# Optimization experiments

Hardware: AMD Instinct MI355X
Metric: run time of the kernel (lower is better)

The kernel has to match this reference:

```python
import jax, jax.numpy as jnp
import numpy as np

B, E, H, W = 8, 1024, 16, 1024
DH = E // H


def setup_inputs() -> dict:
    key = jax.random.key(0)
    ks = jax.random.split(key, 5)
    scale = E ** (-0.5)
    return {
        "x": jax.random.normal(ks[0], (3, B, E, W), dtype=jnp.float32),
        "L_Q": jax.random.normal(ks[1], (E, E), dtype=jnp.float32) * scale,
        "L_K": jax.random.normal(ks[2], (E, E), dtype=jnp.float32) * scale,
        "L_V": jax.random.normal(ks[3], (E, E), dtype=jnp.float32) * scale,
        "dense_M": jax.random.normal(ks[4], (E, E), dtype=jnp.float32) * scale,
        "dense_b": jnp.zeros((E, 1), dtype=jnp.float32),
    }


def reference(x, L_Q, L_K, L_V, dense_M, dense_b):
    # x: [3, B, E, W], channels-first sequences (dropout layers are identity in eval)
    K, Q, V = x[0], x[1], x[2]                      # each [B, E, W]
    K = jnp.einsum('ef,bfw->bew', L_K, K)
    Q = jnp.einsum('ef,bfw->bew', L_Q, Q)
    V = jnp.einsum('ef,bfw->bew', L_V, V)
    Kv = K.reshape(B, H, DH, W)
    Qv = Q.reshape(B, H, DH, W)
    Vv = V.reshape(B, H, DH, W)
    # Q_v^T @ K_v -> [B, H, Wq, Wk]
    scores = jnp.einsum('bhdq,bhdk->bhqk', Qv, Kv)
    # causal_factor = tril(-inf, diag=-1): -inf strictly below the diagonal (q > k)
    qi = jnp.arange(W)[:, None]
    ki = jnp.arange(W)[None, :]
    scores = jnp.where(qi > ki, -jnp.inf, scores)
    # softmax over the QUERY axis (-2), post-scaled by E^-0.5 (non-standard)
    attn = jax.nn.softmax(scores, axis=-2) * (E ** (-0.5))
    # V_v @ scores: contract over the query axis -> [B, H, DH, Wk]
    out = jnp.einsum('bhdq,bhqk->bhdk', Vv, attn).reshape(B, E, W)
    # dense output projection: M @ out + b (bias broadcasts over W)
    return jnp.einsum('ef,bfw->bew', dense_M, out) + dense_b
```

## Files before the change

### kernel.cpp

```cpp
#include <hip/hip_runtime.h>

typedef float  f4  __attribute__((ext_vector_type(4)));
typedef short  s8v __attribute__((ext_vector_type(8)));
typedef unsigned short u16;
typedef u16 us4 __attribute__((ext_vector_type(4)));

constexpr int En  = 1024;
constexpr int Wn  = 1024;
constexpr int Bn  = 8;
constexpr int Hn  = 16;
constexpr int DHn = 64;

__device__ inline u16 bf16rn(float x) {
    unsigned u = __float_as_uint(x);
    return (u16)((u + 0x7FFFu + ((u >> 16) & 1u)) >> 16);
}
__device__ inline float bf16tof(u16 h) { return __uint_as_float(((unsigned)h) << 16); }

#define GLD_LDS16(gp, lp) __builtin_amdgcn_global_load_lds(                      \
    (const __attribute__((address_space(1))) void*)(gp),                         \
    (__attribute__((address_space(3))) void*)(lp), 16, 0, 0)

__global__ void split_plain4(const float* __restrict__ p0,
                             const float* __restrict__ p1,
                             const float* __restrict__ p2,
                             const float* __restrict__ p3,
                             u16* __restrict__ base) {
    const int z = blockIdx.y;
    const float* in = (z == 0) ? p0 : (z == 1) ? p1 : (z == 2) ? p2 : p3;
    u16* hi = base + (size_t)(2 * z) * En * En;
    u16* lo = base + (size_t)(2 * z + 1) * En * En;
    int i = blockIdx.x * blockDim.x + threadIdx.x;
    f4 v = ((const f4*)in)[i];
    us4 h, l;
    #pragma unroll
    for (int k = 0; k < 4; ++k) {
        u16 hh = bf16rn(v[k]);
        h[k] = hh;
        l[k] = bf16rn(v[k] - bf16tof(hh));
    }
    ((us4*)hi)[i] = h;
    ((us4*)lo)[i] = l;
}

__global__ __launch_bounds__(256)
void split_t(const float* __restrict__ in, u16* __restrict__ hi,
             u16* __restrict__ lo) {
    __shared__ float T[32][33];
    const int z = blockIdx.z;
    const size_t zo = (size_t)z * En * Wn;
    const int r0 = blockIdx.y * 32, c0 = blockIdx.x * 32;
    const int t = threadIdx.x;
    const int row = t >> 3, c4 = (t & 7) << 2;

    f4 v = *(const f4*)&in[zo + (size_t)(r0 + row) * Wn + c0 + c4];
    T[row][c4 + 0] = v[0]; T[row][c4 + 1] = v[1];
    T[row][c4 + 2] = v[2]; T[row][c4 + 3] = v[3];
    __syncthreads();

    const int oc = row, r4 = c4;
    us4 h, l;
    #pragma unroll
    for (int i = 0; i < 4; ++i) {
        float x = T[r4 + i][oc];
        u16 hh = bf16rn(x);
        h[i] = hh;
        l[i] = bf16rn(x - bf16tof(hh));
    }
    *(us4*)&hi[zo + (size_t)(c0 + oc) * En + r0 + r4] = h;
    *(us4*)&lo[zo + (size_t)(c0 + oc) * En + r0 + r4] = l;
}

template<int MODE>
__global__ __launch_bounds__(256, 3)
void gemm_mfma(const u16* __restrict__ Ah,  const u16* __restrict__ Al,
               const u16* __restrict__ Bth, const u16* __restrict__ Btl,
               float* __restrict__ Yf, u16* __restrict__ Yh, u16* __restrict__ Yl,
               const float* __restrict__ bias) {
    __shared__ u16 AsH[4096], AsL[4096], BsH[4096], BsL[4096];

    const int z  = blockIdx.z;
    const size_t zB = (size_t)z * Wn * En;
    const int e0 = blockIdx.y * 128, n0 = blockIdx.x * 128;
    const int t = threadIdx.x, lane = t & 63, wave = t >> 6;
    const int q = lane >> 4, r = lane & 15;
    const int m_off = (wave & 1) * 64, n_off = (wave >> 1) * 64;

    f4 acc[4][4];
    #pragma unroll
    for (int i = 0; i < 4; ++i)
        #pragma unroll
        for (int j = 0; j < 4; ++j) { acc[i][j][0]=0; acc[i][j][1]=0; acc[i][j][2]=0; acc[i][j][3]=0; }

    for (int kb = 0; kb < En; kb += 32) {
        __syncthreads();
        #pragma unroll
        for (int it = 0; it < 2; ++it) {
            const int id = t + 256 * it;
            const int u = id >> 3;
            const int p = (id & 7) ^ (u & 7);
            const int m = 2 * u + (p >> 2), g = p & 3;
            const size_t colA = (size_t)kb + 8 * g;
            const u16* ga_h = Ah  + (size_t)(e0 + m) * En + colA;
            const u16* ga_l = Al  + (size_t)(e0 + m) * En + colA;
            const u16* gb_h = Bth + zB + (size_t)(n0 + m) * En + colA;
            const u16* gb_l = Btl + zB + (size_t)(n0 + m) * En + colA;
            GLD_LDS16(ga_h, &AsH[id * 8]);
            GLD_LDS16(ga_l, &AsL[id * 8]);
            GLD_LDS16(gb_h, &BsH[id * 8]);
            GLD_LDS16(gb_l, &BsL[id * 8]);
        }
        __syncthreads();

        s8v aH[4], aL[4];
        #pragma unroll
        for (int i = 0; i < 4; ++i) {
            const int Ra = m_off + 16 * i + r;
            const int sa = ((((Ra & 1) << 2) | q) ^ ((Ra >> 1) & 7));
            const int ai = ((Ra >> 1) * 8 + sa) * 8;
            aH[i] = *(const s8v*)&AsH[ai];
            aL[i] = *(const s8v*)&AsL[ai];
        }
        #pragma unroll
        for (int j = 0; j < 4; ++j) {
            const int Rb = n_off + 16 * j + r;
            const int sb = ((((Rb & 1) << 2) | q) ^ ((Rb >> 1) & 7));
            const int bi = ((Rb >> 1) * 8 + sb) * 8;
            s8v bH = *(const s8v*)&BsH[bi];
            s8v bL = *(const s8v*)&BsL[bi];
            #pragma unroll
            for (int i = 0; i < 4; ++i) {
                acc[i][j] = __builtin_amdgcn_mfma_f32_16x16x32_bf16(aH[i], bH, acc[i][j], 0, 0, 0);
                acc[i][j] = __builtin_amdgcn_mfma_f32_16x16x32_bf16(aH[i], bL, acc[i][j], 0, 0, 0);
                acc[i][j] = __builtin_amdgcn_mfma_f32_16x16x32_bf16(aL[i], bH, acc[i][j], 0, 0, 0);
            }
        }
    }

    if constexpr (MODE == 0) {
        const size_t zY = (size_t)z * En * Wn;
        #pragma unroll
        for (int i = 0; i < 4; ++i) {
            #pragma unroll
            for (int reg = 0; reg < 4; ++reg) {
                const int e = e0 + m_off + 16 * i + q * 4 + reg;
                const float bv = bias ? bias[e] : 0.0f;
                #pragma unroll
                for (int j = 0; j < 4; ++j) {
                    const int w = n0 + n_off + 16 * j + r;
                    Yf[zY + (size_t)e * Wn + w] = acc[i][j][reg] + bv;
                }
            }
        }
    }
    if constexpr (MODE == 1) {
        #pragma unroll
        for (int i = 0; i < 4; ++i) {
            const int e_base = e0 + m_off + 16 * i + q * 4;
            const int bh_e = z * Hn + (e_base >> 6);
            const int d0 = e_base & 63;
            #pragma unroll
            for (int j = 0; j < 4; ++j) {
                const int w = n0 + n_off + 16 * j + r;
                us4 h, l;
                #pragma unroll
                for (int reg = 0; reg < 4; ++reg) {
                    float x = acc[i][j][reg];
                    u16 hh = bf16rn(x);
                    h[reg] = hh;
                    l[reg] = bf16rn(x - bf16tof(hh));
                }
                const size_t o = ((size_t)bh_e * Wn + w) * 64 + d0;
                *(us4*)&Yh[o] = h;
                *(us4*)&Yl[o] = l;
            }
        }
    }
    if constexpr (MODE == 2) {
        #pragma unroll
        for (int i = 0; i < 4; ++i) {
            #pragma unroll
            for (int reg = 0; reg < 4; ++reg) {
                const int e = e0 + m_off + 16 * i + q * 4 + reg;
                const int bh_e = z * Hn + (e >> 6);
                const int d = e & 63;
                const size_t ro = ((size_t)bh_e * 64 + d) * Wn;
                #pragma unroll
                for (int j = 0; j < 4; ++j) {
                    const int w = n0 + n_off + 16 * j + r;
                    Yh[ro + w] = bf16rn(acc[i][j][reg]);
                }
            }
        }
    }
}

__global__ __launch_bounds__(256, 3)
void attn_mfma3(const u16* __restrict__ QTh, const u16* __restrict__ QTl,
                const u16* __restrict__ KTh, const u16* __restrict__ KTl,
                const u16* __restrict__ Vb,  u16* __restrict__ AoTh,
                u16* __restrict__ AoTl) {
    __shared__ u16 QsH[4096], QsL[4096], Vs[4096];
    __shared__ u16 PT[4][16][72];

    const int id   = blockIdx.x;
    const int rest = id >> 3;
    const int kb   = 15 - (rest & 15);
    const int bh   = (id & 7) + 8 * (rest >> 4);

    const int t = threadIdx.x, lane = t & 63, wave = t >> 6;
    const int r = lane & 15, quad = lane >> 4;
    const int k0 = kb * 64;
    const int kcol = k0 + wave * 16 + r;
    u16 (*pt)[72] = PT[wave];

    const size_t qkb = (size_t)bh * Wn * 64;
    const size_t vbb = (size_t)bh * 64 * Wn;

    s8v kH[2], kL[2];
    #pragma unroll
    for (int s = 0; s < 2; ++s) {
        const size_t a = qkb + (size_t)kcol * 64 + s * 32 + quad * 8;
        kH[s] = *(const s8v*)&KTh[a];
        kL[s] = *(const s8v*)&KTl[a];
    }

    f4 o[4];
    #pragma unroll
    for (int i = 0; i < 4; ++i) { o[i][0]=0; o[i][1]=0; o[i][2]=0; o[i][3]=0; }
    float m = -1e30f, l = 0.0f;

    const int c0 = t,       row0 = c0 >> 3, p0 = (c0 & 7) ^ (row0 & 7);
    const int c1 = t + 256, row1 = c1 >> 3, p1 = (c1 & 7) ^ (row1 & 7);

    s8v Aqh0, Aqh1, Aql0, Aql1, Av0, Av1;
    s8v Bqh0, Bqh1, Bql0, Bql1, Bv0, Bv1;

    auto ld = [&](int q0, s8v& qh0, s8v& qh1, s8v& ql0, s8v& ql1,
                  s8v& v0, s8v& v1) {
        const size_t g = qkb + (size_t)q0 * 64;
        qh0 = *(const s8v*)&QTh[g + (size_t)row0 * 64 + p0 * 8];
        ql0 = *(const s8v*)&QTl[g + (size_t)row0 * 64 + p0 * 8];
        v0  = *(const s8v*)&Vb[vbb + (size_t)row0 * Wn + q0 + p0 * 8];
        qh1 = *(const s8v*)&QTh[g + (size_t)row1 * 64 + p1 * 8];
        ql1 = *(const s8v*)&QTl[g + (size_t)row1 * 64 + p1 * 8];
        v1  = *(const s8v*)&Vb[vbb + (size_t)row1 * Wn + q0 + p1 * 8];
    };
    auto wr = [&](s8v& qh0, s8v& qh1, s8v& ql0, s8v& ql1, s8v& v0, s8v& v1) {
        *(s8v*)&QsH[c0 * 8] = qh0; *(s8v*)&QsL[c0 * 8] = ql0; *(s8v*)&Vs[c0 * 8] = v0;
        *(s8v*)&QsH[c1 * 8] = qh1; *(s8v*)&QsL[c1 * 8] = ql1; *(s8v*)&Vs[c1 * 8] = v1;
    };

    auto compute = [&](int q0) {
        f4 sacc[4];
        #pragma unroll
        for (int mt = 0; mt < 4; ++mt) { sacc[mt][0]=0; sacc[mt][1]=0; sacc[mt][2]=0; sacc[mt][3]=0; }
        #pragma unroll
        for (int s = 0; s < 2; ++s) {
            const int sw = (((s * 4 + quad) ^ (r & 7)) << 3);
            #pragma unroll
            for (int mt = 0; mt < 4; ++mt) {
                const int a = (16 * mt + r) * 64 + sw;
                s8v qh = *(const s8v*)&QsH[a];
                s8v ql = *(const s8v*)&QsL[a];
                sacc[mt] = __builtin_amdgcn_mfma_f32_16x16x32_bf16(qh, kH[s], sacc[mt], 0, 0, 0);
                sacc[mt] = __builtin_amdgcn_mfma_f32_16x16x32_bf16(qh, kL[s], sacc[mt], 0, 0, 0);
                sacc[mt] = __builtin_amdgcn_mfma_f32_16x16x32_bf16(ql, kH[s], sacc[mt], 0, 0, 0);
            }
        }
        if (q0 == k0) {
            const int klocal = wave * 16 + r;
            #pragma unroll
            for (int mt = 0; mt < 4; ++mt)
                #pragma unroll
                for (int reg = 0; reg < 4; ++reg)
                    if (16 * mt + quad * 4 + reg > klocal) sacc[mt][reg] = -1e30f;
        }
        float tm = -1e30f;
        #pragma unroll
        for (int mt = 0; mt < 4; ++mt)
            #pragma unroll
            for (int reg = 0; reg < 4; ++reg) tm = fmaxf(tm, sacc[mt][reg]);
        tm = fmaxf(tm, __shfl_xor(tm, 16));
        tm = fmaxf(tm, __shfl_xor(tm, 32));
        if (!__all(tm - m <= 8.0f)) {
            const float mnew  = fmaxf(m, tm);
            const float alpha = __expf(m - mnew);
            l *= alpha;
            #pragma unroll
            for (int i = 0; i < 4; ++i) {
                o[i][0] *= alpha; o[i][1] *= alpha;
                o[i][2] *= alpha; o[i][3] *= alpha;
            }
            m = mnew;
        }
        float ps = 0.0f;
        #pragma unroll
        for (int mt = 0; mt < 4; ++mt) {
            us4 pk;
            #pragma unroll
            for (int reg = 0; reg < 4; ++reg) {
                float p = __expf(sacc[mt][reg] - m);
                ps += p;
                pk[reg] = bf16rn(p);
            }
            *(us4*)&pt[r][16 * mt + quad * 4] = pk;
        }
        ps += __shfl_xor(ps, 16);
        ps += __shfl_xor(ps, 32);
        l += ps;
        #pragma unroll
        for (int s = 0; s < 2; ++s) {
            const int sw = (((s * 4 + quad) ^ (r & 7)) << 3);
            s8v pf = *(const s8v*)&pt[r][s * 32 + quad * 8];
            #pragma unroll
            for (int i = 0; i < 4; ++i) {
                s8v vf = *(const s8v*)&Vs[(16 * i + r) * 64 + sw];
                o[i] = __builtin_amdgcn_mfma_f32_16x16x32_bf16(vf, pf, o[i], 0, 0, 0);
            }
        }
    };

    ld(0, Aqh0, Aqh1, Aql0, Aql1, Av0, Av1);
    int q0 = 0;
    for (;;) {
        __syncthreads();
        wr(Aqh0, Aqh1, Aql0, Aql1, Av0, Av1);
        __syncthreads();
        if (q0 + 64 <= k0) ld(q0 + 64, Bqh0, Bqh1, Bql0, Bql1, Bv0, Bv1);
        compute(q0);
        q0 += 64;
        if (q0 > k0) break;
        __syncthreads();
        wr(Bqh0, Bqh1, Bql0, Bql1, Bv0, Bv1);
        __syncthreads();
        if (q0 + 64 <= k0) ld(q0 + 64, Aqh0, Aqh1, Aql0, Aql1, Av0, Av1);
        compute(q0);
        q0 += 64;
        if (q0 > k0) break;
    }

    const float inv = 1.0f / (l * 32.0f);
    const size_t ob0 = (size_t)(bh >> 4) * ((size_t)Wn * En) +
                       (size_t)kcol * En + (bh & 15) * 64 + quad * 4;
    #pragma unroll
    for (int i = 0; i < 4; ++i) {
        us4 h, lo4;
        #pragma unroll
        for (int reg = 0; reg < 4; ++reg) {
            float x = o[i][reg] * inv;
            u16 hh = bf16rn(x);
            h[reg] = hh;
            lo4[reg] = bf16rn(x - bf16tof(hh));
        }
        *(us4*)&AoTh[ob0 + 16 * i] = h;
        *(us4*)&AoTl[ob0 + 16 * i] = lo4;
    }
}

__global__ __launch_bounds__(256, 2)
void gemm128(const float* __restrict__ L, const float* __restrict__ X,
             float* __restrict__ Y, const float* __restrict__ bias) {
    __shared__ float As[16][132];
    __shared__ float Bs[16][132];

    const int bz = blockIdx.z;
    const float* Xb = X + (size_t)bz * En * Wn;
    float*       Yb = Y + (size_t)bz * En * Wn;
    const int e0 = blockIdx.y * 128;
    const int w0 = blockIdx.x * 128;
    const int t  = threadIdx.x;
    const int tx = t & 15, ty = t >> 4;
    const int la_e = t >> 2, la_f = (t & 3) << 2;
    const int lb_f = t >> 5, lb_w = (t & 31) << 2;

    float acc[2][2][4][4] = {};

    for (int f0 = 0; f0 < En; f0 += 16) {
        f4 a0 = *(const f4*)&L [(size_t)(e0 + la_e)      * En + f0 + la_f];
        f4 a1 = *(const f4*)&L [(size_t)(e0 + la_e + 64) * En + f0 + la_f];
        f4 b0 = *(const f4*)&Xb[(size_t)(f0 + lb_f)      * Wn + w0 + lb_w];
        f4 b1 = *(const f4*)&Xb[(size_t)(f0 + lb_f + 8)  * Wn + w0 + lb_w];
        __syncthreads();
        As[la_f + 0][la_e] = a0[0]; As[la_f + 1][la_e] = a0[1];
        As[la_f + 2][la_e] = a0[2]; As[la_f + 3][la_e] = a0[3];
        As[la_f + 0][la_e + 64] = a1[0]; As[la_f + 1][la_e + 64] = a1[1];
        As[la_f + 2][la_e + 64] = a1[2]; As[la_f + 3][la_e + 64] = a1[3];
        *(f4*)&Bs[lb_f    ][lb_w] = b0;
        *(f4*)&Bs[lb_f + 8][lb_w] = b1;
        __syncthreads();
        #pragma unroll
        for (int kk = 0; kk < 16; ++kk) {
            f4 av0 = *(f4*)&As[kk][ty * 4];
            f4 av1 = *(f4*)&As[kk][ty * 4 + 64];
            f4 bv0 = *(f4*)&Bs[kk][tx * 4];
            f4 bv1 = *(f4*)&Bs[kk][tx * 4 + 64];
            #pragma unroll
            for (int i = 0; i < 4; ++i)
                #pragma unroll
                for (int j = 0; j < 4; ++j) {
                    acc[0][0][i][j] = fmaf(av0[i], bv0[j], acc[0][0][i][j]);
                    acc[0][1][i][j] = fmaf(av0[i], bv1[j], acc[0][1][i][j]);
                    acc[1][0][i][j] = fmaf(av1[i], bv0[j], acc[1][0][i][j]);
                    acc[1][1][i][j] = fmaf(av1[i], bv1[j], acc[1][1][i][j]);
                }
        }
    }

    #pragma unroll
    for (int eh = 0; eh < 2; ++eh)
        #pragma unroll
        for (int i = 0; i < 4; ++i) {
            const int e = e0 + eh * 64 + ty * 4 + i;
            const float bv = bias ? bias[e] : 0.0f;
            #pragma unroll
            for (int wh = 0; wh < 2; ++wh) {
                f4 v;
                #pragma unroll
                for (int j = 0; j < 4; ++j) v[j] = acc[eh][wh][i][j] + bv;
                *(f4*)&Yb[(size_t)e * Wn + w0 + wh * 64 + tx * 4] = v;
            }
        }
}

__global__ __launch_bounds__(256, 2)
void attn64(const float* __restrict__ Qg, const float* __restrict__ Kg,
            const float* __restrict__ Vg, float* __restrict__ Og) {
    __shared__ float Ks[64][68];
    __shared__ float QP[64][68];
    __shared__ float Vt[64][68];
    __shared__ float mArr[64], lArr[64], alphaArr[64];
    __shared__ float red[4][64];

    const int kb = blockIdx.x, h = blockIdx.y, b = blockIdx.z;
    const size_t base = ((size_t)b * En + (size_t)h * DHn) * Wn;
    const float* Qp = Qg + base;
    const float* Kp = Kg + base;
    const float* Vp = Vg + base;
    float*       Op = Og + base;

    const int t  = threadIdx.x;
    const int tx = t & 15, ty = t >> 4;
    const int lr = t >> 4;
    const int lc = (t & 15) << 2;
    const int k0 = kb * 64;
    const int kc = t & 63, qg = t >> 6;

    #pragma unroll
    for (int r = 0; r < 4; ++r)
        *(f4*)&Ks[lr + r * 16][lc] =
            *(const f4*)&Kp[(size_t)(lr + r * 16) * Wn + k0 + lc];
    if (t < 64) { mArr[t] = -1e30f; lArr[t] = 0.0f; }
    float acc[4][4] = {};
    __syncthreads();

    for (int q0 = 0; q0 <= k0; q0 += 64) {
        #pragma unroll
        for (int r = 0; r < 4; ++r) {
            const int d = lr + r * 16;
            f4 qv = *(const f4*)&Qp[(size_t)d * Wn + q0 + lc];
            f4 vv = *(const f4*)&Vp[(size_t)d * Wn + q0 + lc];
            *(f4*)&QP[d][lc] = qv;
            Vt[lc + 0][d] = vv[0]; Vt[lc + 1][d] = vv[1];
            Vt[lc + 2][d] = vv[2]; Vt[lc + 3][d] = vv[3];
        }
        __syncthreads();

        float s[4][4] = {};
        #pragma unroll 4
        for (int d = 0; d < 64; ++d) {
            f4 kv = *(f4*)&Ks[d][tx * 4];
            f4 q2 = *(f4*)&QP[d][ty * 4];
            #pragma unroll
            for (int i = 0; i < 4; ++i)
                #pragma unroll
                for (int j = 0; j < 4; ++j)
                    s[i][j] = fmaf(q2[i], kv[j], s[i][j]);
        }
        if (q0 == k0) {
            #pragma unroll
            for (int i = 0; i < 4; ++i)
                #pragma unroll
                for (int j = 0; j < 4; ++j)
                    if (ty * 4 + i > tx * 4 + j) s[i][j] = -1e30f;
        }
        __syncthreads();
        #pragma unroll
        for (int i = 0; i < 4; ++i) {
            f4 v;
            #pragma unroll
            for (int j = 0; j < 4; ++j) v[j] = s[i][j];
            *(f4*)&QP[ty * 4 + i][tx * 4] = v;
        }
        __syncthreads();

        float sv[16];
        float lm = -1e30f;
        #pragma unroll
        for (int r = 0; r < 16; ++r) {
            sv[r] = QP[qg * 16 + r][kc];
            lm = fmaxf(lm, sv[r]);
        }
        red[qg][kc] = lm;
        __syncthreads();
        const float mt    = fmaxf(fmaxf(red[0][kc], red[1][kc]),
                                  fmaxf(red[2][kc], red[3][kc]));
        const float mprev = mArr[kc];
        const float mnew  = fmaxf(mprev, mt);
        float psum = 0.0f;
        #pragma unroll
        for (int r = 0; r < 16; ++r) {
            const float p = __expf(sv[r] - mnew);
            psum += p;
            QP[qg * 16 + r][kc] = p;
        }
        __syncthreads();
        red[qg][kc] = psum;
        __syncthreads();
        if (qg == 0) {
            const float alpha = __expf(mprev - mnew);
            lArr[kc] = lArr[kc] * alpha +
                       (red[0][kc] + red[1][kc] + red[2][kc] + red[3][kc]);
            mArr[kc]     = mnew;
            alphaArr[kc] = alpha;
        }
        __syncthreads();

        f4 al = *(f4*)&alphaArr[tx * 4];
        #pragma unroll
        for (int i = 0; i < 4; ++i)
            #pragma unroll
            for (int j = 0; j < 4; ++j)
                acc[i][j] *= al[j];
        #pragma unroll 4
        for (int q = 0; q < 64; ++q) {
            f4 pv = *(f4*)&QP[q][tx * 4];
            f4 v2 = *(f4*)&Vt[q][ty * 4];
            #pragma unroll
            for (int i = 0; i < 4; ++i)
                #pragma unroll
                for (int j = 0; j < 4; ++j)
                    acc[i][j] = fmaf(v2[i], pv[j], acc[i][j]);
        }
        __syncthreads();
    }

    f4 linv = *(f4*)&lArr[tx * 4];
    #pragma unroll
    for (int j = 0; j < 4; ++j) linv[j] = 1.0f / (linv[j] * 32.0f);
    #pragma unroll
    for (int i = 0; i < 4; ++i) {
        f4 v;
        #pragma unroll
        for (int j = 0; j < 4; ++j) v[j] = acc[i][j] * linv[j];
        *(f4*)&Op[(size_t)(ty * 4 + i) * Wn + k0 + tx * 4] = v;
    }
}

extern "C" void kernel_launch(void* const* d_in, const int* in_sizes, int n_in,
                              void* d_out, int out_size, void* d_ws, size_t ws_size,
                              hipStream_t stream) {
    const float* x    = (const float*)d_in[0];
    const float* L_Q  = (const float*)d_in[1];
    const float* L_K  = (const float*)d_in[2];
    const float* L_V  = (const float*)d_in[3];
    const float* M    = (const float*)d_in[4];
    const float* bias = (const float*)d_in[5];
    float* out = (float*)d_out;

    const size_t mat   = (size_t)Bn * En * Wn;
    const size_t matB  = mat * 4;
    const size_t lmatB = (size_t)En * En * 2;
    const size_t need  = 8 * lmatB + 4 * matB + matB / 2 + matB;

    if (ws_size >= need) {
        char* w = (char*)d_ws;
        u16*  Lsp = (u16*)w;
        char* XT  = w + 8 * lmatB;
        char* R1  = XT + matB;
        char* R2  = R1 + matB;
        char* R3  = R2 + matB;
        char* R4  = R3 + matB / 2;

        u16* LKh = Lsp + 0 * (lmatB / 2); u16* LKl = Lsp + 1 * (lmatB / 2);
        u16* LQh = Lsp + 2 * (lmatB / 2); u16* LQl = Lsp + 3 * (lmatB / 2);
        u16* LVh = Lsp + 4 * (lmatB / 2); u16* LVl = Lsp + 5 * (lmatB / 2);
        u16* Mh  = Lsp + 6 * (lmatB / 2); u16* Ml  = Lsp + 7 * (lmatB / 2);

        u16* XT_H = (u16*)XT;  u16* XT_L = (u16*)(XT + matB / 2);
        u16* KT_h = (u16*)R1;  u16* KT_l = (u16*)(R1 + matB / 2);
        u16* QT_h = (u16*)R2;  u16* QT_l = (u16*)(R2 + matB / 2);
        u16* Vb   = (u16*)R3;
        u16* AoTh = (u16*)R4;  u16* AoTl = (u16*)(R4 + matB / 2);

        const int n4L = En * En / 4;
        hipLaunchKernelGGL(split_plain4, dim3(n4L / 256, 4), dim3(256), 0, stream,
                           L_K, L_Q, L_V, M, Lsp);

        dim3 gt(Wn / 32, En / 32, Bn), bt(256);
        dim3 gg(Wn / 128, En / 128, Bn), bg(256);

        hipLaunchKernelGGL(split_t, gt, bt, 0, stream, x + 0 * mat, XT_H, XT_L);
        hipLaunchKernelGGL(HIP_KERNEL_NAME(gemm_mfma<1>), gg, bg, 0, stream,
                           LKh, LKl, XT_H, XT_L, (float*)nullptr, KT_h, KT_l, (const float*)nullptr);
        hipLaunchKernelGGL(split_t, gt, bt, 0, stream, x + 1 * mat, XT_H, XT_L);
        hipLaunchKernelGGL(HIP_KERNEL_NAME(gemm_mfma<1>), gg, bg, 0, stream,
                           LQh, LQl, XT_H, XT_L, (float*)nullptr, QT_h, QT_l, (const float*)nullptr);
        hipLaunchKernelGGL(split_t, gt, bt, 0, stream, x + 2 * mat, XT_H, XT_L);
        hipLaunchKernelGGL(HIP_KERNEL_NAME(gemm_mfma<2>), gg, bg, 0, stream,
                           LVh, LVl, XT_H, XT_L, (float*)nullptr, Vb, (u16*)nullptr, (const float*)nullptr);

        hipLaunchKernelGGL(attn_mfma3, dim3(2048), dim3(256), 0, stream,
                           QT_h, QT_l, KT_h, KT_l, Vb, AoTh, AoTl);

        hipLaunchKernelGGL(HIP_KERNEL_NAME(gemm_mfma<0>), gg, bg, 0, stream,
                           Mh, Ml, AoTh, AoTl, out, (u16*)nullptr, (u16*)nullptr, bias);
    } else {
        float* ws = (float*)d_ws;
        float* Kp = ws;
        float* Qp = ws + mat;
        float* Vp = ws + 2 * mat;
        float* Ao = ws + 3 * mat;

        dim3 gg(Wn / 128, En / 128, Bn), blk(256);
        hipLaunchKernelGGL(gemm128, gg, blk, 0, stream, L_K, x + 0 * mat, Kp, (const float*)nullptr);
        hipLaunchKernelGGL(gemm128, gg, blk, 0, stream, L_Q, x + 1 * mat, Qp, (const float*)nullptr);
        hipLaunchKernelGGL(gemm128, gg, blk, 0, stream, L_V, x + 2 * mat, Vp, (const float*)nullptr);

        dim3 ga(Wn / 64, Hn, Bn);
        hipLaunchKernelGGL(attn64, ga, blk, 0, stream, Qp, Kp, Vp, Ao);

        hipLaunchKernelGGL(gemm128, gg, blk, 0, stream, M, Ao, out, bias);
    }
}
```

Baseline: 463.7 us.

## Double-buffer LDS tiles in MFMA GEMM to overlap global loads with compute

The split-bf16 MFMA GEMM now keeps two LDS buffers per operand. At the top of each k-iteration it issues the direct-to-LDS global loads for the next k-tile, then runs the MFMAs on the current tile, so memory latency can hide behind compute. It also drops one of the two barriers per iteration. The cost is double the LDS per block, so launch bounds fall from 3 to 2 blocks per CU and occupancy drops. The overlap may be lost if the compiler adds a vmcnt wait before the LDS reads.

```diff
diff --git a/kernel.cpp b/kernel.cpp
--- a/kernel.cpp
+++ b/kernel.cpp
@@ -72,12 +72,12 @@
 }
 
 template<int MODE>
-__global__ __launch_bounds__(256, 3)
+__global__ __launch_bounds__(256, 2)
 void gemm_mfma(const u16* __restrict__ Ah,  const u16* __restrict__ Al,
                const u16* __restrict__ Bth, const u16* __restrict__ Btl,
                float* __restrict__ Yf, u16* __restrict__ Yh, u16* __restrict__ Yl,
                const float* __restrict__ bias) {
-    __shared__ u16 AsH[4096], AsL[4096], BsH[4096], BsL[4096];
+    __shared__ u16 AsH[2][4096], AsL[2][4096], BsH[2][4096], BsL[2][4096];
 
     const int z  = blockIdx.z;
     const size_t zB = (size_t)z * Wn * En;
@@ -92,25 +92,26 @@
         #pragma unroll
         for (int j = 0; j < 4; ++j) { acc[i][j][0]=0; acc[i][j][1]=0; acc[i][j][2]=0; acc[i][j][3]=0; }
 
-    for (int kb = 0; kb < En; kb += 32) {
-        __syncthreads();
+    auto stage = [&](int kb, int buf) {
         #pragma unroll
         for (int it = 0; it < 2; ++it) {
             const int id = t + 256 * it;
-            const int u = id >> 3;
-            const int p = (id & 7) ^ (u & 7);
-            const int m = 2 * u + (p >> 2), g = p & 3;
+            const int u  = id >> 3;
+            const int p  = (id & 7) ^ (u & 7);
+            const int mr = 2 * u + (p >> 2), g = p & 3;
             const size_t colA = (size_t)kb + 8 * g;
-            const u16* ga_h = Ah  + (size_t)(e0 + m) * En + colA;
-            const u16* ga_l = Al  + (size_t)(e0 + m) * En + colA;
-            const u16* gb_h = Bth + zB + (size_t)(n0 + m) * En + colA;
-            const u16* gb_l = Btl + zB + (size_t)(n0 + m) * En + colA;
-            GLD_LDS16(ga_h, &AsH[id * 8]);
-            GLD_LDS16(ga_l, &AsL[id * 8]);
-            GLD_LDS16(gb_h, &BsH[id * 8]);
-            GLD_LDS16(gb_l, &BsL[id * 8]);
-        }
-        __syncthreads();
+            GLD_LDS16(Ah  + (size_t)(e0 + mr) * En + colA, &AsH[buf][id * 8]);
+            GLD_LDS16(Al  + (size_t)(e0 + mr) * En + colA, &AsL[buf][id * 8]);
+            GLD_LDS16(Bth + zB + (size_t)(n0 + mr) * En + colA, &BsH[buf][id * 8]);
+            GLD_LDS16(Btl + zB + (size_t)(n0 + mr) * En + colA, &BsL[buf][id * 8]);
+        }
+    };
+
+    stage(0, 0);
+    int cur = 0;
+    for (int kb = 0; kb < En; kb += 32) {
+        __syncthreads();
+        if (kb + 32 < En) stage(kb + 32, cur ^ 1);
 
         s8v aH[4], aL[4];
         #pragma unroll
@@ -118,16 +119,16 @@
             const int Ra = m_off + 16 * i + r;
             const int sa = ((((Ra & 1) << 2) | q) ^ ((Ra >> 1) & 7));
             const int ai = ((Ra >> 1) * 8 + sa) * 8;
-            aH[i] = *(const s8v*)&AsH[ai];
-            aL[i] = *(const s8v*)&AsL[ai];
+            aH[i] = *(const s8v*)&AsH[cur][ai];
+            aL[i] = *(const s8v*)&AsL[cur][ai];
         }
         #pragma unroll
         for (int j = 0; j < 4; ++j) {
             const int Rb = n_off + 16 * j + r;
             const int sb = ((((Rb & 1) << 2) | q) ^ ((Rb >> 1) & 7));
             const int bi = ((Rb >> 1) * 8 + sb) * 8;
-            s8v bH = *(const s8v*)&BsH[bi];
-            s8v bL = *(const s8v*)&BsL[bi];
+            s8v bH = *(const s8v*)&BsH[cur][bi];
+            s8v bL = *(const s8v*)&BsL[cur][bi];
             #pragma unroll
             for (int i = 0; i < 4; ++i) {
                 acc[i][j] = __builtin_amdgcn_mfma_f32_16x16x32_bf16(aH[i], bH, acc[i][j], 0, 0, 0);
@@ -135,6 +136,7 @@
                 acc[i][j] = __builtin_amdgcn_mfma_f32_16x16x32_bf16(aL[i], bH, acc[i][j], 0, 0, 0);
             }
         }
+        cur ^= 1;
     }
 
     if constexpr (MODE == 0) {
```

Result: no change. 467.4 us (+0.8%).
